# Optimization experiments

Measured on AMD Instinct MI355X. Metric: run time of the kernel, lower is better.

The kernel has to match this reference:

```python
import jax, jax.numpy as jnp
import numpy as np

N = 20000
E = 320000
IN_F = 128
HEADS = 8
OUT_F = 32
NEG_SLOPE = 0.2


def setup_inputs() -> dict:
    key = jax.random.key(0)
    k = jax.random.split(key, 8)
    x = jax.random.normal(k[0], (N, IN_F), dtype=jnp.float32)
    edge_index = jax.random.randint(k[1], (2, E), 0, N, dtype=jnp.int32)
    # Linear weights stored torch-style: [out, in]
    scale = 1.0 / np.sqrt(IN_F)
    W = jax.random.normal(k[2], (HEADS * OUT_F, IN_F), dtype=jnp.float32) * scale
    W1 = jax.random.normal(k[3], (HEADS * OUT_F, IN_F), dtype=jnp.float32) * scale
    W2 = jax.random.normal(k[4], (HEADS * OUT_F, IN_F), dtype=jnp.float32) * scale
    att = jax.random.normal(k[5], (1, HEADS, OUT_F), dtype=jnp.float32) * 0.1
    bias = jnp.zeros((HEADS * OUT_F,), dtype=jnp.float32)
    return {"x": x, "edge_index": edge_index, "W": W, "W1": W1, "W2": W2,
            "att": att, "bias": bias}


def reference(x, edge_index, W, W1, W2, att, bias):
    n, heads, out_f = x.shape[0], att.shape[1], att.shape[2]
    src, dst = edge_index[0], edge_index[1]

    # Node projections: [N, H, F]
    h_src = (x @ W1.T).reshape(n, heads, out_f)
    h_dst = (x @ W2.T).reshape(n, heads, out_f)
    values = (x @ W.T).reshape(n, heads, out_f)

    # Edge-wise GATv2 logits: a^T LeakyReLU(W1 h_i + W2 h_j)  -> [E, H]
    att_input = jax.nn.leaky_relu(h_src[src] + h_dst[dst], negative_slope=NEG_SLOPE)
    logits = jnp.einsum('ehf,hf->eh', att_input, att[0])

    # Segment softmax over incoming edges of each dst node (stable).
    seg_max = jax.ops.segment_max(logits, dst, num_segments=n)  # [N, H]
    exp_l = jnp.exp(logits - seg_max[dst])
    denom = jax.ops.segment_sum(exp_l, dst, num_segments=n)     # [N, H]
    weights = exp_l / denom[dst]                                # [E, H]

    # Weighted aggregation of source values into dst nodes.
    weighted = weights[:, :, None] * values[src]                # [E, H, F]
    out = jax.ops.segment_sum(weighted, dst, num_segments=n)    # [N, H, F]

    out = out.reshape(n, heads * out_f) + bias
    return out
```

## Files before the change

### kernel.cpp

```cpp
#include <hip/hip_runtime.h>
#include <math.h>

#define NN 20000
#define EE 320000
#define KF 128
#define HO 256
#define CAP 96

typedef __attribute__((ext_vector_type(8))) short short8;
typedef __attribute__((ext_vector_type(4))) float f32x4;

static __device__ __forceinline__ unsigned short f2bf(float f) {
    union { float f; unsigned u; } v; v.f = f;
    unsigned u = v.u;
    u += 0x7fffu + ((u >> 16) & 1u);
    return (unsigned short)(u >> 16);
}
static __device__ __forceinline__ float bf2f(unsigned short b) {
    union { unsigned u; float f; } v; v.u = ((unsigned)b) << 16;
    return v.f;
}

__global__ __launch_bounds__(256) void prep_kernel(
    const float* __restrict__ x, const float* __restrict__ W0,
    const float* __restrict__ W1, const float* __restrict__ W2,
    unsigned short* __restrict__ xb, unsigned short* __restrict__ wb,
    int* __restrict__ cursor)
{
    const int b = blockIdx.x;
    const int t = threadIdx.x;
    if (b < 96) {
        const int m = b >> 5;
        const float* __restrict__ Wm = (m == 0) ? W0 : (m == 1) ? W1 : W2;
        int idx = (b & 31) * 1024 + t * 4;
        float4 v = *(const float4*)(Wm + idx);
        ushort4 o;
        o.x = f2bf(v.x); o.y = f2bf(v.y); o.z = f2bf(v.z); o.w = f2bf(v.w);
        *(ushort4*)(wb + (size_t)m * 32768 + idx) = o;
    } else if (b < 2596) {
        size_t i = (size_t)(b - 96) * 1024 + t * 4;
        float4 v = *(const float4*)(x + i);
        ushort4 o;
        o.x = f2bf(v.x); o.y = f2bf(v.y); o.z = f2bf(v.z); o.w = f2bf(v.w);
        *(ushort4*)(xb + i) = o;
    } else {
        int i = (b - 2596) * 256 + t;
        if (i < NN) cursor[i] = 0;
    }
}

__global__ void scatter_kernel(const int* __restrict__ ei, int* __restrict__ cursor,
                               int* __restrict__ csr_src) {
    int e = blockIdx.x * blockDim.x + threadIdx.x;
    if (e < EE) {
        int s = ei[e];
        int d = ei[EE + e];
        int pos = atomicAdd(&cursor[d], 1);
        if (pos < CAP) csr_src[d * CAP + pos] = s;
    }
}

__global__ __launch_bounds__(256, 4) void proj_kernel(
    const unsigned short* __restrict__ xb, const unsigned short* __restrict__ wb,
    unsigned short* __restrict__ hv, unsigned short* __restrict__ hdst)
{
    const int m = blockIdx.y;
    const unsigned short* __restrict__ Wm = wb + (size_t)m * 32768;
    unsigned short* __restrict__ dst = (m == 0) ? (hv + 256) : (m == 1) ? hv : hdst;
    const int stride = (m == 2) ? 256 : 512;

    const int w    = threadIdx.x >> 6;
    const int lane = threadIdx.x & 63;
    const int lr   = lane & 15;
    const int q    = lane >> 4;
    const int cb   = w * 64;

    short8 Bf[4][4];
#pragma unroll
    for (int nt = 0; nt < 4; ++nt)
#pragma unroll
        for (int ks = 0; ks < 4; ++ks)
            Bf[nt][ks] = *(const short8*)(Wm + (size_t)(cb + nt * 16 + lr) * KF + ks * 32 + q * 8);

    const int rb = blockIdx.x * 64;

#pragma unroll
    for (int it = 0; it < 4; ++it) {
        const int r0 = rb + it * 16;

        short8 Af[4];
        const int arow = r0 + lr;
#pragma unroll
        for (int ks = 0; ks < 4; ++ks) {
            Af[ks] = (short8){0,0,0,0,0,0,0,0};
            if (arow < NN)
                Af[ks] = *(const short8*)(xb + (size_t)arow * KF + ks * 32 + q * 8);
        }

        f32x4 acc[4];
#pragma unroll
        for (int nt = 0; nt < 4; ++nt) acc[nt] = (f32x4){0.f, 0.f, 0.f, 0.f};

#pragma unroll
        for (int ks = 0; ks < 4; ++ks)
#pragma unroll
            for (int nt = 0; nt < 4; ++nt)
                acc[nt] = __builtin_amdgcn_mfma_f32_16x16x32_bf16(Af[ks], Bf[nt][ks], acc[nt], 0, 0, 0);

#pragma unroll
        for (int nt = 0; nt < 4; ++nt) {
#pragma unroll
            for (int r = 0; r < 4; ++r) {
                const int row = r0 + q * 4 + r;
                if (row < NN)
                    dst[(size_t)row * stride + cb + nt * 16 + lr] = f2bf(acc[nt][r]);
            }
        }
    }
}

__global__ __launch_bounds__(128) void gat_kernel(
    const unsigned short* __restrict__ hv, const unsigned short* __restrict__ hdst,
    const float* __restrict__ att, const float* __restrict__ bias,
    const int* __restrict__ cursor, const int* __restrict__ csr_src,
    float* __restrict__ out)
{
    const int w    = threadIdx.x >> 6;
    const int d    = blockIdx.x * 2 + w;
    const int lane = threadIdx.x & 63;
    const int col  = lane * 4;

    const float4 a4 = *(const float4*)(att + col);
    const float4 b4 = *(const float4*)(bias + col);
    const ushort4 hd4 = *(const ushort4*)(hdst + (size_t)d * HO + col);
    const float hd0 = bf2f(hd4.x), hd1 = bf2f(hd4.y), hd2 = bf2f(hd4.z), hd3 = bf2f(hd4.w);

    int deg = cursor[d];
    if (deg > CAP) deg = CAP;

    int sreg = (lane < deg) ? csr_src[d * CAP + lane] : 0;

    float l = 0.f;
    float o0 = 0.f, o1 = 0.f, o2 = 0.f, o3 = 0.f;

#define EDGE_CALC(HV, VV)                                                     \
    {                                                                         \
        float z0 = bf2f(HV.x) + hd0, z1 = bf2f(HV.y) + hd1;                   \
        float z2 = bf2f(HV.z) + hd2, z3 = bf2f(HV.w) + hd3;                   \
        z0 = fmaxf(z0, 0.2f * z0); z1 = fmaxf(z1, 0.2f * z1);                 \
        z2 = fmaxf(z2, 0.2f * z2); z3 = fmaxf(z3, 0.2f * z3);                 \
        float p = fmaf(a4.x, z0, a4.y * z1) + fmaf(a4.z, z2, a4.w * z3);      \
        p += __shfl_xor(p, 1); p += __shfl_xor(p, 2); p += __shfl_xor(p, 4);  \
        const float e = __expf(p);                                            \
        l += e;                                                               \
        o0 = fmaf(e, bf2f(VV.x), o0);                                         \
        o1 = fmaf(e, bf2f(VV.y), o1);                                         \
        o2 = fmaf(e, bf2f(VV.z), o2);                                         \
        o3 = fmaf(e, bf2f(VV.w), o3);                                         \
    }

    const int nfast = (deg < 64) ? deg : 64;
    int i = 0;
    for (; i + 4 <= nfast; i += 4) {
        const int s0 = __shfl(sreg, i);
        const int s1 = __shfl(sreg, i + 1);
        const int s2 = __shfl(sreg, i + 2);
        const int s3 = __shfl(sreg, i + 3);
        const unsigned short* p0 = hv + (size_t)s0 * 512 + col;
        const unsigned short* p1 = hv + (size_t)s1 * 512 + col;
        const unsigned short* p2 = hv + (size_t)s2 * 512 + col;
        const unsigned short* p3 = hv + (size_t)s3 * 512 + col;
        const ushort4 hv0 = *(const ushort4*)p0;
        const ushort4 vv0 = *(const ushort4*)(p0 + 256);
        const ushort4 hv1 = *(const ushort4*)p1;
        const ushort4 vv1 = *(const ushort4*)(p1 + 256);
        const ushort4 hv2 = *(const ushort4*)p2;
        const ushort4 vv2 = *(const ushort4*)(p2 + 256);
        const ushort4 hv3 = *(const ushort4*)p3;
        const ushort4 vv3 = *(const ushort4*)(p3 + 256);
        EDGE_CALC(hv0, vv0);
        EDGE_CALC(hv1, vv1);
        EDGE_CALC(hv2, vv2);
        EDGE_CALC(hv3, vv3);
    }
    for (; i < nfast; ++i) {
        const int s0 = __shfl(sreg, i);
        const unsigned short* p0 = hv + (size_t)s0 * 512 + col;
        const ushort4 hv0 = *(const ushort4*)p0;
        const ushort4 vv0 = *(const ushort4*)(p0 + 256);
        EDGE_CALC(hv0, vv0);
    }
    for (int j = 64; j < deg; ++j) {
        const int s0 = csr_src[d * CAP + j];
        const unsigned short* p0 = hv + (size_t)s0 * 512 + col;
        const ushort4 hv0 = *(const ushort4*)p0;
        const ushort4 vv0 = *(const ushort4*)(p0 + 256);
        EDGE_CALC(hv0, vv0);
    }
#undef EDGE_CALC

    const float inv = (deg > 0) ? 1.f / l : 0.f;
    float4 res;
    res.x = o0 * inv + b4.x;
    res.y = o1 * inv + b4.y;
    res.z = o2 * inv + b4.z;
    res.w = o3 * inv + b4.w;
    *(float4*)(out + (size_t)d * HO + col) = res;
}

extern "C" void kernel_launch(void* const* d_in, const int* in_sizes, int n_in,
                              void* d_out, int out_size, void* d_ws, size_t ws_size,
                              hipStream_t stream) {
    const float* x    = (const float*)d_in[0];
    const int*   ei   = (const int*)d_in[1];
    const float* W0   = (const float*)d_in[2];
    const float* W1   = (const float*)d_in[3];
    const float* W2   = (const float*)d_in[4];
    const float* att  = (const float*)d_in[5];
    const float* bias = (const float*)d_in[6];
    float* out = (float*)d_out;

    char* p = (char*)d_ws;
    unsigned short* hv   = (unsigned short*)p; p += (size_t)NN * 512 * 2;
    unsigned short* hdst = (unsigned short*)p; p += (size_t)NN * HO * 2;
    unsigned short* xb   = (unsigned short*)p; p += (size_t)NN * KF * 2;
    unsigned short* wb   = (unsigned short*)p; p += (size_t)3 * 32768 * 2;
    int* cursor  = (int*)p; p += (size_t)NN * sizeof(int);
    int* csr_src = (int*)p; p += (size_t)NN * CAP * sizeof(int);

    prep_kernel<<<2675, 256, 0, stream>>>(x, W0, W1, W2, xb, wb, cursor);
    scatter_kernel<<<(EE + 255) / 256, 256, 0, stream>>>(ei, cursor, csr_src);
    proj_kernel<<<dim3(313, 3), 256, 0, stream>>>(xb, wb, hv, hdst);
    gat_kernel<<<NN / 2, 128, 0, stream>>>(hv, hdst, att, bias, cursor, csr_src, out);
}
```

Before: 161.6 us.

## Split wavefront halves across two edges per step with 16-byte gathers

The GAT aggregation kernel now has each half of the wavefront process a different edge, with each lane loading 8 bf16 values (16 bytes) instead of 4. The per-head dot-product reduction needs one fewer shuffle, and the two halves' partial sums are combined with a cross-half shuffle at the end. Padding edges are masked to zero. Separately, the projection kernel prefetches the next 16-row A tile while computing the current one, and its occupancy hint is lowered from 4 to 3 to give it more registers. The aim is wider memory transactions and more gather parallelism per wavefront, at the cost of extra registers and some wasted work on odd-degree nodes.

```diff
diff --git a/kernel.cpp b/kernel.cpp
--- a/kernel.cpp
+++ b/kernel.cpp
@@ -60,7 +60,7 @@
     }
 }
 
-__global__ __launch_bounds__(256, 4) void proj_kernel(
+__global__ __launch_bounds__(256, 3) void proj_kernel(
     const unsigned short* __restrict__ xb, const unsigned short* __restrict__ wb,
     unsigned short* __restrict__ hv, unsigned short* __restrict__ hdst)
 {
@@ -84,17 +84,30 @@
 
     const int rb = blockIdx.x * 64;
 
-#pragma unroll
-    for (int it = 0; it < 4; ++it) {
-        const int r0 = rb + it * 16;
-
-        short8 Af[4];
-        const int arow = r0 + lr;
+    short8 Af[4];
+    {
+        const int arow = rb + lr;
 #pragma unroll
         for (int ks = 0; ks < 4; ++ks) {
             Af[ks] = (short8){0,0,0,0,0,0,0,0};
             if (arow < NN)
                 Af[ks] = *(const short8*)(xb + (size_t)arow * KF + ks * 32 + q * 8);
+        }
+    }
+
+#pragma unroll
+    for (int it = 0; it < 4; ++it) {
+        const int r0 = rb + it * 16;
+
+        short8 An[4];
+        if (it < 3) {
+            const int arow = r0 + 16 + lr;
+#pragma unroll
+            for (int ks = 0; ks < 4; ++ks) {
+                An[ks] = (short8){0,0,0,0,0,0,0,0};
+                if (arow < NN)
+                    An[ks] = *(const short8*)(xb + (size_t)arow * KF + ks * 32 + q * 8);
+            }
         }
 
         f32x4 acc[4];
@@ -115,6 +128,11 @@
                 if (row < NN)
                     dst[(size_t)row * stride + cb + nt * 16 + lr] = f2bf(acc[nt][r]);
             }
+        }
+
+        if (it < 3) {
+#pragma unroll
+            for (int ks = 0; ks < 4; ++ks) Af[ks] = An[ks];
         }
     }
 }
@@ -128,12 +146,20 @@
     const int w    = threadIdx.x >> 6;
     const int d    = blockIdx.x * 2 + w;
     const int lane = threadIdx.x & 63;
-    const int col  = lane * 4;
-
-    const float4 a4 = *(const float4*)(att + col);
-    const float4 b4 = *(const float4*)(bias + col);
-    const ushort4 hd4 = *(const ushort4*)(hdst + (size_t)d * HO + col);
-    const float hd0 = bf2f(hd4.x), hd1 = bf2f(hd4.y), hd2 = bf2f(hd4.z), hd3 = bf2f(hd4.w);
+    const int half = lane >> 5;
+    const int sub  = lane & 31;
+    const int c8   = sub * 8;
+
+    float a[8], hd[8];
+    {
+        const float4 aa = *(const float4*)(att + c8);
+        const float4 ab = *(const float4*)(att + c8 + 4);
+        a[0] = aa.x; a[1] = aa.y; a[2] = aa.z; a[3] = aa.w;
+        a[4] = ab.x; a[5] = ab.y; a[6] = ab.z; a[7] = ab.w;
+        const short8 h8 = *(const short8*)(hdst + (size_t)d * HO + c8);
+#pragma unroll
+        for (int j = 0; j < 8; ++j) hd[j] = bf2f((unsigned short)h8[j]);
+    }
 
     int deg = cursor[d];
     if (deg > CAP) deg = CAP;
@@ -141,71 +167,80 @@
     int sreg = (lane < deg) ? csr_src[d * CAP + lane] : 0;
 
     float l = 0.f;
-    float o0 = 0.f, o1 = 0.f, o2 = 0.f, o3 = 0.f;
-
-#define EDGE_CALC(HV, VV)                                                     \
+    float o[8] = {0.f, 0.f, 0.f, 0.f, 0.f, 0.f, 0.f, 0.f};
+
+#define EDGE_CALC(HS, VS, MASK)                                               \
     {                                                                         \
-        float z0 = bf2f(HV.x) + hd0, z1 = bf2f(HV.y) + hd1;                   \
-        float z2 = bf2f(HV.z) + hd2, z3 = bf2f(HV.w) + hd3;                   \
-        z0 = fmaxf(z0, 0.2f * z0); z1 = fmaxf(z1, 0.2f * z1);                 \
-        z2 = fmaxf(z2, 0.2f * z2); z3 = fmaxf(z3, 0.2f * z3);                 \
-        float p = fmaf(a4.x, z0, a4.y * z1) + fmaf(a4.z, z2, a4.w * z3);      \
-        p += __shfl_xor(p, 1); p += __shfl_xor(p, 2); p += __shfl_xor(p, 4);  \
-        const float e = __expf(p);                                            \
+        float p = 0.f;                                                        \
+        _Pragma("unroll")                                                     \
+        for (int j = 0; j < 8; ++j) {                                         \
+            float z = bf2f((unsigned short)HS[j]) + hd[j];                    \
+            z = fmaxf(z, 0.2f * z);                                           \
+            p = fmaf(a[j], z, p);                                             \
+        }                                                                     \
+        p += __shfl_xor(p, 1);                                                \
+        p += __shfl_xor(p, 2);                                                \
+        const float e = __expf(p) * (MASK);                                   \
         l += e;                                                               \
-        o0 = fmaf(e, bf2f(VV.x), o0);                                         \
-        o1 = fmaf(e, bf2f(VV.y), o1);                                         \
-        o2 = fmaf(e, bf2f(VV.z), o2);                                         \
-        o3 = fmaf(e, bf2f(VV.w), o3);                                         \
+        _Pragma("unroll")                                                     \
+        for (int j = 0; j < 8; ++j)                                           \
+            o[j] = fmaf(e, bf2f((unsigned short)VS[j]), o[j]);                \
     }
 
     const int nfast = (deg < 64) ? deg : 64;
+    const int npair = (nfast + 1) >> 1;
     int i = 0;
-    for (; i + 4 <= nfast; i += 4) {
-        const int s0 = __shfl(sreg, i);
-        const int s1 = __shfl(sreg, i + 1);
-        const int s2 = __shfl(sreg, i + 2);
-        const int s3 = __shfl(sreg, i + 3);
-        const unsigned short* p0 = hv + (size_t)s0 * 512 + col;
-        const unsigned short* p1 = hv + (size_t)s1 * 512 + col;
-        const unsigned short* p2 = hv + (size_t)s2 * 512 + col;
-        const unsigned short* p3 = hv + (size_t)s3 * 512 + col;
-        const ushort4 hv0 = *(const ushort4*)p0;
-        const ushort4 vv0 = *(const ushort4*)(p0 + 256);
-        const ushort4 hv1 = *(const ushort4*)p1;
-        const ushort4 vv1 = *(const ushort4*)(p1 + 256);
-        const ushort4 hv2 = *(const ushort4*)p2;
-        const ushort4 vv2 = *(const ushort4*)(p2 + 256);
-        const ushort4 hv3 = *(const ushort4*)p3;
-        const ushort4 vv3 = *(const ushort4*)(p3 + 256);
-        EDGE_CALC(hv0, vv0);
-        EDGE_CALC(hv1, vv1);
-        EDGE_CALC(hv2, vv2);
-        EDGE_CALC(hv3, vv3);
-    }
-    for (; i < nfast; ++i) {
-        const int s0 = __shfl(sreg, i);
-        const unsigned short* p0 = hv + (size_t)s0 * 512 + col;
-        const ushort4 hv0 = *(const ushort4*)p0;
-        const ushort4 vv0 = *(const ushort4*)(p0 + 256);
-        EDGE_CALC(hv0, vv0);
+    for (; i + 2 <= npair; i += 2) {
+        const int i0 = 2 * i + half;
+        const int i1 = 2 * (i + 1) + half;
+        const int s0 = __shfl(sreg, i0);
+        const int s1 = __shfl(sreg, i1);
+        const unsigned short* p0 = hv + (size_t)s0 * 512 + c8;
+        const unsigned short* p1 = hv + (size_t)s1 * 512 + c8;
+        const short8 h0 = *(const short8*)p0;
+        const short8 v0 = *(const short8*)(p0 + 256);
+        const short8 h1 = *(const short8*)p1;
+        const short8 v1 = *(const short8*)(p1 + 256);
+        const float m0 = (i0 < deg) ? 1.f : 0.f;
+        const float m1 = (i1 < deg) ? 1.f : 0.f;
+        EDGE_CALC(h0, v0, m0);
+        EDGE_CALC(h1, v1, m1);
+    }
+    for (; i < npair; ++i) {
+        const int i0 = 2 * i + half;
+        const int s0 = __shfl(sreg, i0);
+        const unsigned short* p0 = hv + (size_t)s0 * 512 + c8;
+        const short8 h0 = *(const short8*)p0;
+        const short8 v0 = *(const short8*)(p0 + 256);
+        const float m0 = (i0 < deg) ? 1.f : 0.f;
+        EDGE_CALC(h0, v0, m0);
     }
     for (int j = 64; j < deg; ++j) {
         const int s0 = csr_src[d * CAP + j];
-        const unsigned short* p0 = hv + (size_t)s0 * 512 + col;
-        const ushort4 hv0 = *(const ushort4*)p0;
-        const ushort4 vv0 = *(const ushort4*)(p0 + 256);
-        EDGE_CALC(hv0, vv0);
+        const unsigned short* p0 = hv + (size_t)s0 * 512 + c8;
+        const short8 h0 = *(const short8*)p0;
+        const short8 v0 = *(const short8*)(p0 + 256);
+        const float m0 = (half == 0) ? 1.f : 0.f;
+        EDGE_CALC(h0, v0, m0);
     }
 #undef EDGE_CALC
 
+    l += __shfl_xor(l, 32);
+#pragma unroll
+    for (int j = 0; j < 8; ++j) o[j] += __shfl_xor(o[j], 32);
+
     const float inv = (deg > 0) ? 1.f / l : 0.f;
+    const float s0 = half ? o[4] : o[0];
+    const float s1 = half ? o[5] : o[1];
+    const float s2 = half ? o[6] : o[2];
+    const float s3 = half ? o[7] : o[3];
+    const float4 bb = *(const float4*)(bias + c8 + half * 4);
     float4 res;
-    res.x = o0 * inv + b4.x;
-    res.y = o1 * inv + b4.y;
-    res.z = o2 * inv + b4.z;
-    res.w = o3 * inv + b4.w;
-    *(float4*)(out + (size_t)d * HO + col) = res;
+    res.x = s0 * inv + bb.x;
+    res.y = s1 * inv + bb.y;
+    res.z = s2 * inv + bb.z;
+    res.w = s3 * inv + bb.w;
+    *(float4*)(out + (size_t)d * HO + c8 + half * 4) = res;
 }
 
 extern "C" void kernel_launch(void* const* d_in, const int* in_sizes, int n_in,
```

Measured after the change: 161.7 us. Within noise of the previous version (+0.1%).
